# Optimization experiments

Hardware: AMD Instinct MI355X
Metric: run time of the kernel (lower is better)

The kernel has to match this reference:

```python
import jax, jax.numpy as jnp
import numpy as np

N = 50000        # nodes
E = 1_600_000    # edges (avg degree 32)
IN = 8           # in_channels
OUT = 64         # out_channels / hidden
K = 2            # Chebyshev order


def setup_inputs() -> dict:
    key = jax.random.key(0)
    ks = jax.random.split(key, 16)
    w = lambda k, s: (jax.random.normal(k, s, jnp.float32) * 0.05)
    inp = {
        "x": jax.random.normal(ks[0], (N, IN), jnp.float32),
        "H": jax.random.normal(ks[1], (N, OUT), jnp.float32),
        "edge_index": jax.random.randint(ks[2], (2, E), 0, N, dtype=jnp.int64),
    }
    names = [("z_x", IN), ("z_h", OUT), ("r_x", IN), ("r_h", OUT), ("c_x", IN), ("c_h", OUT)]
    for i, (nm, d) in enumerate(names):
        inp["W_" + nm] = w(ks[3 + 2 * i], (K, d, OUT))
        inp["b_" + nm] = w(ks[4 + 2 * i], (OUT,))
    return inp


def _cheb(x, W, b, row, col, norm):
    # PyG-style ChebConv with lambda_max=2: L_hat = -D^{-1/2} A D^{-1/2}
    # Tx0 = x; Tx1 = L_hat x; Tx_k = 2 L_hat Tx_{k-1} - Tx_{k-2}
    out = x @ W[0]
    Tx0 = x
    Tx1 = jax.ops.segment_sum(norm[:, None] * x[col], row, num_segments=N)
    out = out + Tx1 @ W[1]
    for k in range(2, W.shape[0]):
        Tx2 = 2.0 * jax.ops.segment_sum(norm[:, None] * Tx1[col], row, num_segments=N) - Tx0
        out = out + Tx2 @ W[k]
        Tx0, Tx1 = Tx1, Tx2
    return out + b


def reference(x, H, edge_index, W_z_x, b_z_x, W_z_h, b_z_h, W_r_x, b_r_x,
              W_r_h, b_r_h, W_c_x, b_c_x, W_c_h, b_c_h):
    row, col = edge_index[0], edge_index[1]
    deg = jax.ops.segment_sum(jnp.ones((E,), x.dtype), row, num_segments=N)
    dinv = jnp.where(deg > 0, 1.0 / jnp.sqrt(jnp.where(deg > 0, deg, 1.0)), 0.0)
    norm = -dinv[row] * dinv[col]  # sym-normalized, negated adjacency (L - I)

    Z = jax.nn.sigmoid(_cheb(x, W_z_x, b_z_x, row, col, norm)
                       + _cheb(H, W_z_h, b_z_h, row, col, norm))
    R = jax.nn.sigmoid(_cheb(x, W_r_x, b_r_x, row, col, norm)
                       + _cheb(H, W_r_h, b_r_h, row, col, norm))
    C = jnp.tanh(_cheb(x, W_c_x, b_c_x, row, col, norm)
                 + _cheb(R * H, W_c_h, b_c_h, row, col, norm))
    return Z * H + (1.0 - Z) * C
```

## Files before the change

### kernel.cpp

```cpp
#include <hip/hip_runtime.h>
#include <math.h>

#define IN_CH 8
#define OUT_CH 64

__global__ void deg_kernel(const int* __restrict__ row, int* __restrict__ deg, int E) {
    int i = blockIdx.x * blockDim.x + threadIdx.x;
    if (i < E) atomicAdd(&deg[row[i]], 1);
}

__global__ void dinv_kernel(const int* __restrict__ deg, float* __restrict__ dinv, int N) {
    int i = blockIdx.x * blockDim.x + threadIdx.x;
    if (i < N) {
        int d = deg[i];
        dinv[i] = (d > 0) ? rsqrtf((float)d) : 0.f;
    }
}

__global__ void scan_kernel(const int* __restrict__ deg, int* __restrict__ rowptr,
                            int* __restrict__ cursor, int N) {
    __shared__ int s_wave[17];
    __shared__ int s_running;
    int tid = threadIdx.x;
    int lane = tid & 63, wid = tid >> 6;
    if (tid == 0) s_running = 0;
    __syncthreads();
    for (int base = 0; base < N; base += 1024) {
        int i = base + tid;
        int v = (i < N) ? deg[i] : 0;
        int incl = v;
#pragma unroll
        for (int off = 1; off < 64; off <<= 1) {
            int t = __shfl_up(incl, off, 64);
            if (lane >= off) incl += t;
        }
        if (lane == 63) s_wave[wid] = incl;
        __syncthreads();
        if (wid == 0) {
            int wv = (lane < 16) ? s_wave[lane] : 0;
            int winc = wv;
#pragma unroll
            for (int off = 1; off < 16; off <<= 1) {
                int t = __shfl_up(winc, off, 64);
                if (lane >= off) winc += t;
            }
            if (lane < 16) s_wave[lane] = winc - wv;
            if (lane == 15) s_wave[16] = winc;
        }
        __syncthreads();
        int run = s_running;
        int excl = run + s_wave[wid] + incl - v;
        if (i < N) { rowptr[i] = excl; cursor[i] = excl; }
        __syncthreads();
        if (tid == 0) s_running = run + s_wave[16];
        __syncthreads();
    }
    if (tid == 0) rowptr[N] = s_running;
}

__global__ void bucket_kernel(const int* __restrict__ ei, const float* __restrict__ dinv,
                              int* __restrict__ cursor, int* __restrict__ col_s,
                              float* __restrict__ norm_s, int E) {
    int e = blockIdx.x * blockDim.x + threadIdx.x;
    if (e >= E) return;
    int r = ei[e];
    int c = ei[E + e];
    float nm = -dinv[r] * dinv[c];
    int pos = atomicAdd(&cursor[r], 1);
    col_s[pos] = c;
    norm_s[pos] = nm;
}

__global__ void gather64_kernel(const int* __restrict__ rowptr, const int* __restrict__ col_s,
                                const float* __restrict__ norm_s, const float* __restrict__ src,
                                float* __restrict__ dst, int N) {
    int n = blockIdx.x * (blockDim.x >> 6) + (threadIdx.x >> 6);
    int o = threadIdx.x & 63;
    if (n >= N) return;
    int beg = rowptr[n], end = rowptr[n + 1];
    float acc = 0.f;
#pragma unroll 4
    for (int j = beg; j < end; ++j) {
        int c = col_s[j];
        float nm = norm_s[j];
        acc = fmaf(nm, src[(long long)c * OUT_CH + o], acc);
    }
    dst[(long long)n * OUT_CH + o] = acc;
}

__global__ void gather8_kernel(const int* __restrict__ rowptr, const int* __restrict__ col_s,
                               const float* __restrict__ norm_s, const float* __restrict__ src,
                               float* __restrict__ dst, int N) {
    int n = blockIdx.x * (blockDim.x >> 6) + (threadIdx.x >> 6);
    int lane = threadIdx.x & 63;
    int g = lane >> 3;
    int o = lane & 7;
    if (n >= N) return;
    int beg = rowptr[n], end = rowptr[n + 1];
    float acc = 0.f;
    for (int j = beg + g; j < end; j += 8) {
        int c = col_s[j];
        float nm = norm_s[j];
        acc = fmaf(nm, src[(long long)c * IN_CH + o], acc);
    }
#pragma unroll
    for (int m = 8; m < 64; m <<= 1) acc += __shfl_xor(acc, m, 64);
    if (g == 0) dst[(long long)n * IN_CH + o] = acc;
}

__device__ __forceinline__ float sigmoidf(float v) { return 1.0f / (1.0f + expf(-v)); }

__global__ void gates_kernel(const float* __restrict__ x, const float* __restrict__ H,
                             const float* __restrict__ Lx, const float* __restrict__ LH,
                             const float* __restrict__ Wzx, const float* __restrict__ bzx,
                             const float* __restrict__ Wzh, const float* __restrict__ bzh,
                             const float* __restrict__ Wrx, const float* __restrict__ brx,
                             const float* __restrict__ Wrh, const float* __restrict__ brh,
                             float* __restrict__ Z, float* __restrict__ RH, int N) {
    int n = blockIdx.x * (blockDim.x >> 6) + (threadIdx.x >> 6);
    int o = threadIdx.x & 63;
    if (n >= N) return;
    float accZ = bzx[o] + bzh[o];
    float accR = brx[o] + brh[o];
    const float* xr  = x  + (long long)n * IN_CH;
    const float* lxr = Lx + (long long)n * IN_CH;
#pragma unroll
    for (int k = 0; k < IN_CH; ++k) {
        float xv = xr[k], lxv = lxr[k];
        accZ = fmaf(xv,  Wzx[k * 64 + o],       accZ);
        accZ = fmaf(lxv, Wzx[512 + k * 64 + o], accZ);
        accR = fmaf(xv,  Wrx[k * 64 + o],       accR);
        accR = fmaf(lxv, Wrx[512 + k * 64 + o], accR);
    }
    const float* hr  = H  + (long long)n * OUT_CH;
    const float* lhr = LH + (long long)n * OUT_CH;
    for (int k = 0; k < OUT_CH; ++k) {
        float hv = hr[k], lhv = lhr[k];
        accZ = fmaf(hv,  Wzh[k * 64 + o],        accZ);
        accZ = fmaf(lhv, Wzh[4096 + k * 64 + o], accZ);
        accR = fmaf(hv,  Wrh[k * 64 + o],        accR);
        accR = fmaf(lhv, Wrh[4096 + k * 64 + o], accR);
    }
    float z = sigmoidf(accZ);
    float r = sigmoidf(accR);
    Z[(long long)n * 64 + o]  = z;
    RH[(long long)n * 64 + o] = r * hr[o];
}

__global__ void final_kernel(const float* __restrict__ x, const float* __restrict__ H,
                             const float* __restrict__ Lx, const float* __restrict__ RH,
                             const float* __restrict__ LRH,
                             const float* __restrict__ Wcx, const float* __restrict__ bcx,
                             const float* __restrict__ Wch, const float* __restrict__ bch,
                             const float* __restrict__ Z, float* __restrict__ out, int N) {
    int n = blockIdx.x * (blockDim.x >> 6) + (threadIdx.x >> 6);
    int o = threadIdx.x & 63;
    if (n >= N) return;
    float accC = bcx[o] + bch[o];
    const float* xr  = x  + (long long)n * IN_CH;
    const float* lxr = Lx + (long long)n * IN_CH;
#pragma unroll
    for (int k = 0; k < IN_CH; ++k) {
        float xv = xr[k], lxv = lxr[k];
        accC = fmaf(xv,  Wcx[k * 64 + o],       accC);
        accC = fmaf(lxv, Wcx[512 + k * 64 + o], accC);
    }
    const float* rhr  = RH  + (long long)n * OUT_CH;
    const float* lrhr = LRH + (long long)n * OUT_CH;
    for (int k = 0; k < OUT_CH; ++k) {
        float rv = rhr[k], lrv = lrhr[k];
        accC = fmaf(rv,  Wch[k * 64 + o],        accC);
        accC = fmaf(lrv, Wch[4096 + k * 64 + o], accC);
    }
    float c = tanhf(accC);
    float z = Z[(long long)n * 64 + o];
    float h = H[(long long)n * 64 + o];
    out[(long long)n * 64 + o] = z * h + (1.0f - z) * c;
}

extern "C" void kernel_launch(void* const* d_in, const int* in_sizes, int n_in,
                              void* d_out, int out_size, void* d_ws, size_t ws_size,
                              hipStream_t stream) {
    const float* x   = (const float*)d_in[0];
    const float* H   = (const float*)d_in[1];
    const int*   ei  = (const int*)d_in[2];
    const float* Wzx = (const float*)d_in[3];
    const float* bzx = (const float*)d_in[4];
    const float* Wzh = (const float*)d_in[5];
    const float* bzh = (const float*)d_in[6];
    const float* Wrx = (const float*)d_in[7];
    const float* brx = (const float*)d_in[8];
    const float* Wrh = (const float*)d_in[9];
    const float* brh = (const float*)d_in[10];
    const float* Wcx = (const float*)d_in[11];
    const float* bcx = (const float*)d_in[12];
    const float* Wch = (const float*)d_in[13];
    const float* bch = (const float*)d_in[14];

    const int N = in_sizes[0] / IN_CH;
    const int E = in_sizes[2] / 2;

    int*   deg    = (int*)d_ws;
    float* dinv   = (float*)(deg + N);
    int*   rowptr = (int*)(dinv + N);
    int*   col_s  = rowptr + (N + 1);
    float* norm_s = (float*)(col_s + E);
    float* Lx     = norm_s + E;
    float* LH     = Lx + (size_t)N * IN_CH;
    float* Z      = LH + (size_t)N * OUT_CH;
    float* RH     = Z  + (size_t)N * OUT_CH;
    float* LRH    = LH;
    int*   cursor = deg;

    hipMemsetAsync(deg, 0, (size_t)N * sizeof(int), stream);

    const int tb = 256;
    deg_kernel<<<(E + tb - 1) / tb, tb, 0, stream>>>(ei, deg, E);
    dinv_kernel<<<(N + tb - 1) / tb, tb, 0, stream>>>(deg, dinv, N);
    scan_kernel<<<1, 1024, 0, stream>>>(deg, rowptr, cursor, N);
    bucket_kernel<<<(E + tb - 1) / tb, tb, 0, stream>>>(ei, dinv, cursor, col_s, norm_s, E);

    const int nblk = (N + 3) / 4;
    gather8_kernel <<<nblk, tb, 0, stream>>>(rowptr, col_s, norm_s, x, Lx, N);
    gather64_kernel<<<nblk, tb, 0, stream>>>(rowptr, col_s, norm_s, H, LH, N);

    gates_kernel<<<nblk, tb, 0, stream>>>(x, H, Lx, LH, Wzx, bzx, Wzh, bzh,
                                          Wrx, brx, Wrh, brh, Z, RH, N);

    gather64_kernel<<<nblk, tb, 0, stream>>>(rowptr, col_s, norm_s, RH, LRH, N);

    final_kernel<<<nblk, tb, 0, stream>>>(x, H, Lx, RH, LRH, Wcx, bcx, Wch, bch,
                                          Z, (float*)d_out, N);
}
```

Before: 714.5 us.

## Pack edge metadata as int2, broadcast via shuffles, register-block dense gate kernels

Edge column and norm are now stored interleaved as one int2 array. The 64-wide gather loads up to 64 edges' metadata cooperatively, one per lane, and broadcasts each with wave shuffles instead of every lane reloading the same scalars. The gate and final kernels now process 4 nodes per wave: node features are held in registers and broadcast with shuffles, so each weight load is reused across 4 nodes. This trades extra shuffle instructions and register pressure for fewer redundant global and scalar loads.

```diff
diff --git a/kernel.cpp b/kernel.cpp
--- a/kernel.cpp
+++ b/kernel.cpp
@@ -59,38 +59,38 @@
 }
 
 __global__ void bucket_kernel(const int* __restrict__ ei, const float* __restrict__ dinv,
-                              int* __restrict__ cursor, int* __restrict__ col_s,
-                              float* __restrict__ norm_s, int E) {
+                              int* __restrict__ cursor, int2* __restrict__ meta, int E) {
     int e = blockIdx.x * blockDim.x + threadIdx.x;
     if (e >= E) return;
     int r = ei[e];
     int c = ei[E + e];
     float nm = -dinv[r] * dinv[c];
     int pos = atomicAdd(&cursor[r], 1);
-    col_s[pos] = c;
-    norm_s[pos] = nm;
-}
-
-__global__ void gather64_kernel(const int* __restrict__ rowptr, const int* __restrict__ col_s,
-                                const float* __restrict__ norm_s, const float* __restrict__ src,
-                                float* __restrict__ dst, int N) {
+    meta[pos] = make_int2(c, __float_as_int(nm));
+}
+
+__global__ void gather64_kernel(const int* __restrict__ rowptr, const int2* __restrict__ meta,
+                                const float* __restrict__ src, float* __restrict__ dst, int N) {
     int n = blockIdx.x * (blockDim.x >> 6) + (threadIdx.x >> 6);
-    int o = threadIdx.x & 63;
+    int lane = threadIdx.x & 63;
     if (n >= N) return;
     int beg = rowptr[n], end = rowptr[n + 1];
     float acc = 0.f;
+    for (int base = beg; base < end; base += 64) {
+        int cnt = min(end - base, 64);
+        int2 m = meta[base + min(lane, cnt - 1)];
 #pragma unroll 4
-    for (int j = beg; j < end; ++j) {
-        int c = col_s[j];
-        float nm = norm_s[j];
-        acc = fmaf(nm, src[(long long)c * OUT_CH + o], acc);
-    }
-    dst[(long long)n * OUT_CH + o] = acc;
-}
-
-__global__ void gather8_kernel(const int* __restrict__ rowptr, const int* __restrict__ col_s,
-                               const float* __restrict__ norm_s, const float* __restrict__ src,
-                               float* __restrict__ dst, int N) {
+        for (int e = 0; e < cnt; ++e) {
+            int c = __shfl(m.x, e, 64);
+            float nm = __int_as_float(__shfl(m.y, e, 64));
+            acc = fmaf(nm, src[(size_t)c * OUT_CH + lane], acc);
+        }
+    }
+    dst[(size_t)n * OUT_CH + lane] = acc;
+}
+
+__global__ void gather8_kernel(const int* __restrict__ rowptr, const int2* __restrict__ meta,
+                               const float* __restrict__ src, float* __restrict__ dst, int N) {
     int n = blockIdx.x * (blockDim.x >> 6) + (threadIdx.x >> 6);
     int lane = threadIdx.x & 63;
     int g = lane >> 3;
@@ -99,83 +99,131 @@
     int beg = rowptr[n], end = rowptr[n + 1];
     float acc = 0.f;
     for (int j = beg + g; j < end; j += 8) {
-        int c = col_s[j];
-        float nm = norm_s[j];
-        acc = fmaf(nm, src[(long long)c * IN_CH + o], acc);
-    }
-#pragma unroll
-    for (int m = 8; m < 64; m <<= 1) acc += __shfl_xor(acc, m, 64);
-    if (g == 0) dst[(long long)n * IN_CH + o] = acc;
+        int2 m = meta[j];
+        acc = fmaf(__int_as_float(m.y), src[(size_t)m.x * IN_CH + o], acc);
+    }
+#pragma unroll
+    for (int msk = 8; msk < 64; msk <<= 1) acc += __shfl_xor(acc, msk, 64);
+    if (g == 0) dst[(size_t)n * IN_CH + o] = acc;
 }
 
 __device__ __forceinline__ float sigmoidf(float v) { return 1.0f / (1.0f + expf(-v)); }
 
-__global__ void gates_kernel(const float* __restrict__ x, const float* __restrict__ H,
-                             const float* __restrict__ Lx, const float* __restrict__ LH,
-                             const float* __restrict__ Wzx, const float* __restrict__ bzx,
-                             const float* __restrict__ Wzh, const float* __restrict__ bzh,
-                             const float* __restrict__ Wrx, const float* __restrict__ brx,
-                             const float* __restrict__ Wrh, const float* __restrict__ brh,
-                             float* __restrict__ Z, float* __restrict__ RH, int N) {
-    int n = blockIdx.x * (blockDim.x >> 6) + (threadIdx.x >> 6);
-    int o = threadIdx.x & 63;
-    if (n >= N) return;
-    float accZ = bzx[o] + bzh[o];
-    float accR = brx[o] + brh[o];
-    const float* xr  = x  + (long long)n * IN_CH;
-    const float* lxr = Lx + (long long)n * IN_CH;
+__global__ __launch_bounds__(256) void gates_kernel(
+        const float* __restrict__ x, const float* __restrict__ H,
+        const float* __restrict__ Lx, const float* __restrict__ LH,
+        const float* __restrict__ Wzx, const float* __restrict__ bzx,
+        const float* __restrict__ Wzh, const float* __restrict__ bzh,
+        const float* __restrict__ Wrx, const float* __restrict__ brx,
+        const float* __restrict__ Wrh, const float* __restrict__ brh,
+        float* __restrict__ Z, float* __restrict__ RH, int N) {
+    int wid = threadIdx.x >> 6;
+    int lane = threadIdx.x & 63;
+    int n0 = blockIdx.x * 16 + wid * 4;
+
+    float axl[4], hreg[4], lhreg[4], accZ[4], accR[4];
+    float bz = bzx[lane] + bzh[lane];
+    float br = brx[lane] + brh[lane];
+#pragma unroll
+    for (int i = 0; i < 4; ++i) {
+        int n = n0 + i;
+        int nn = (n < N) ? n : 0;
+        axl[i]   = (lane < 8) ? x[(size_t)nn * IN_CH + lane]
+                 : (lane < 16 ? Lx[(size_t)nn * IN_CH + (lane - 8)] : 0.f);
+        hreg[i]  = H[(size_t)nn * OUT_CH + lane];
+        lhreg[i] = LH[(size_t)nn * OUT_CH + lane];
+        accZ[i] = bz;
+        accR[i] = br;
+    }
 #pragma unroll
     for (int k = 0; k < IN_CH; ++k) {
-        float xv = xr[k], lxv = lxr[k];
-        accZ = fmaf(xv,  Wzx[k * 64 + o],       accZ);
-        accZ = fmaf(lxv, Wzx[512 + k * 64 + o], accZ);
-        accR = fmaf(xv,  Wrx[k * 64 + o],       accR);
-        accR = fmaf(lxv, Wrx[512 + k * 64 + o], accR);
-    }
-    const float* hr  = H  + (long long)n * OUT_CH;
-    const float* lhr = LH + (long long)n * OUT_CH;
+        float wz0 = Wzx[k * 64 + lane], wz1 = Wzx[512 + k * 64 + lane];
+        float wr0 = Wrx[k * 64 + lane], wr1 = Wrx[512 + k * 64 + lane];
+#pragma unroll
+        for (int i = 0; i < 4; ++i) {
+            float xv  = __shfl(axl[i], k, 64);
+            float lxv = __shfl(axl[i], k + 8, 64);
+            accZ[i] = fmaf(xv, wz0, fmaf(lxv, wz1, accZ[i]));
+            accR[i] = fmaf(xv, wr0, fmaf(lxv, wr1, accR[i]));
+        }
+    }
+#pragma unroll 8
     for (int k = 0; k < OUT_CH; ++k) {
-        float hv = hr[k], lhv = lhr[k];
-        accZ = fmaf(hv,  Wzh[k * 64 + o],        accZ);
-        accZ = fmaf(lhv, Wzh[4096 + k * 64 + o], accZ);
-        accR = fmaf(hv,  Wrh[k * 64 + o],        accR);
-        accR = fmaf(lhv, Wrh[4096 + k * 64 + o], accR);
-    }
-    float z = sigmoidf(accZ);
-    float r = sigmoidf(accR);
-    Z[(long long)n * 64 + o]  = z;
-    RH[(long long)n * 64 + o] = r * hr[o];
-}
-
-__global__ void final_kernel(const float* __restrict__ x, const float* __restrict__ H,
-                             const float* __restrict__ Lx, const float* __restrict__ RH,
-                             const float* __restrict__ LRH,
-                             const float* __restrict__ Wcx, const float* __restrict__ bcx,
-                             const float* __restrict__ Wch, const float* __restrict__ bch,
-                             const float* __restrict__ Z, float* __restrict__ out, int N) {
-    int n = blockIdx.x * (blockDim.x >> 6) + (threadIdx.x >> 6);
-    int o = threadIdx.x & 63;
-    if (n >= N) return;
-    float accC = bcx[o] + bch[o];
-    const float* xr  = x  + (long long)n * IN_CH;
-    const float* lxr = Lx + (long long)n * IN_CH;
+        float wh0 = Wzh[k * 64 + lane], wh1 = Wzh[4096 + k * 64 + lane];
+        float wr0 = Wrh[k * 64 + lane], wr1 = Wrh[4096 + k * 64 + lane];
+#pragma unroll
+        for (int i = 0; i < 4; ++i) {
+            float hv  = __shfl(hreg[i], k, 64);
+            float lhv = __shfl(lhreg[i], k, 64);
+            accZ[i] = fmaf(hv, wh0, fmaf(lhv, wh1, accZ[i]));
+            accR[i] = fmaf(hv, wr0, fmaf(lhv, wr1, accR[i]));
+        }
+    }
+#pragma unroll
+    for (int i = 0; i < 4; ++i) {
+        int n = n0 + i;
+        if (n < N) {
+            float z = sigmoidf(accZ[i]);
+            float r = sigmoidf(accR[i]);
+            Z[(size_t)n * OUT_CH + lane]  = z;
+            RH[(size_t)n * OUT_CH + lane] = r * hreg[i];
+        }
+    }
+}
+
+__global__ __launch_bounds__(256) void final_kernel(
+        const float* __restrict__ x, const float* __restrict__ H,
+        const float* __restrict__ Lx, const float* __restrict__ RH,
+        const float* __restrict__ LRH,
+        const float* __restrict__ Wcx, const float* __restrict__ bcx,
+        const float* __restrict__ Wch, const float* __restrict__ bch,
+        const float* __restrict__ Z, float* __restrict__ out, int N) {
+    int wid = threadIdx.x >> 6;
+    int lane = threadIdx.x & 63;
+    int n0 = blockIdx.x * 16 + wid * 4;
+
+    float axl[4], rhreg[4], lrhreg[4], accC[4];
+    float bc = bcx[lane] + bch[lane];
+#pragma unroll
+    for (int i = 0; i < 4; ++i) {
+        int n = n0 + i;
+        int nn = (n < N) ? n : 0;
+        axl[i]    = (lane < 8) ? x[(size_t)nn * IN_CH + lane]
+                  : (lane < 16 ? Lx[(size_t)nn * IN_CH + (lane - 8)] : 0.f);
+        rhreg[i]  = RH[(size_t)nn * OUT_CH + lane];
+        lrhreg[i] = LRH[(size_t)nn * OUT_CH + lane];
+        accC[i] = bc;
+    }
 #pragma unroll
     for (int k = 0; k < IN_CH; ++k) {
-        float xv = xr[k], lxv = lxr[k];
-        accC = fmaf(xv,  Wcx[k * 64 + o],       accC);
-        accC = fmaf(lxv, Wcx[512 + k * 64 + o], accC);
-    }
-    const float* rhr  = RH  + (long long)n * OUT_CH;
-    const float* lrhr = LRH + (long long)n * OUT_CH;
+        float wc0 = Wcx[k * 64 + lane], wc1 = Wcx[512 + k * 64 + lane];
+#pragma unroll
+        for (int i = 0; i < 4; ++i) {
+            float xv  = __shfl(axl[i], k, 64);
+            float lxv = __shfl(axl[i], k + 8, 64);
+            accC[i] = fmaf(xv, wc0, fmaf(lxv, wc1, accC[i]));
+        }
+    }
+#pragma unroll 8
     for (int k = 0; k < OUT_CH; ++k) {
-        float rv = rhr[k], lrv = lrhr[k];
-        accC = fmaf(rv,  Wch[k * 64 + o],        accC);
-        accC = fmaf(lrv, Wch[4096 + k * 64 + o], accC);
-    }
-    float c = tanhf(accC);
-    float z = Z[(long long)n * 64 + o];
-    float h = H[(long long)n * 64 + o];
-    out[(long long)n * 64 + o] = z * h + (1.0f - z) * c;
+        float wh0 = Wch[k * 64 + lane], wh1 = Wch[4096 + k * 64 + lane];
+#pragma unroll
+        for (int i = 0; i < 4; ++i) {
+            float rv  = __shfl(rhreg[i], k, 64);
+            float lrv = __shfl(lrhreg[i], k, 64);
+            accC[i] = fmaf(rv, wh0, fmaf(lrv, wh1, accC[i]));
+        }
+    }
+#pragma unroll
+    for (int i = 0; i < 4; ++i) {
+        int n = n0 + i;
+        if (n < N) {
+            float c = tanhf(accC[i]);
+            float z = Z[(size_t)n * OUT_CH + lane];
+            float h = H[(size_t)n * OUT_CH + lane];
+            out[(size_t)n * OUT_CH + lane] = z * h + (1.0f - z) * c;
+        }
+    }
 }
 
 extern "C" void kernel_launch(void* const* d_in, const int* in_sizes, int n_in,
@@ -203,9 +251,8 @@
     int*   deg    = (int*)d_ws;
     float* dinv   = (float*)(deg + N);
     int*   rowptr = (int*)(dinv + N);
-    int*   col_s  = rowptr + (N + 1);
-    float* norm_s = (float*)(col_s + E);
-    float* Lx     = norm_s + E;
+    int2*  meta   = (int2*)(rowptr + (N + 2));
+    float* Lx     = (float*)(meta + E);
     float* LH     = Lx + (size_t)N * IN_CH;
     float* Z      = LH + (size_t)N * OUT_CH;
     float* RH     = Z  + (size_t)N * OUT_CH;
@@ -218,17 +265,19 @@
     deg_kernel<<<(E + tb - 1) / tb, tb, 0, stream>>>(ei, deg, E);
     dinv_kernel<<<(N + tb - 1) / tb, tb, 0, stream>>>(deg, dinv, N);
     scan_kernel<<<1, 1024, 0, stream>>>(deg, rowptr, cursor, N);
-    bucket_kernel<<<(E + tb - 1) / tb, tb, 0, stream>>>(ei, dinv, cursor, col_s, norm_s, E);
-
-    const int nblk = (N + 3) / 4;
-    gather8_kernel <<<nblk, tb, 0, stream>>>(rowptr, col_s, norm_s, x, Lx, N);
-    gather64_kernel<<<nblk, tb, 0, stream>>>(rowptr, col_s, norm_s, H, LH, N);
-
-    gates_kernel<<<nblk, tb, 0, stream>>>(x, H, Lx, LH, Wzx, bzx, Wzh, bzh,
-                                          Wrx, brx, Wrh, brh, Z, RH, N);
-
-    gather64_kernel<<<nblk, tb, 0, stream>>>(rowptr, col_s, norm_s, RH, LRH, N);
-
-    final_kernel<<<nblk, tb, 0, stream>>>(x, H, Lx, RH, LRH, Wcx, bcx, Wch, bch,
-                                          Z, (float*)d_out, N);
-}
+    bucket_kernel<<<(E + tb - 1) / tb, tb, 0, stream>>>(ei, dinv, cursor, meta, E);
+
+    const int nblk4 = (N + 3) / 4;
+    const int nblk16 = (N + 15) / 16;
+
+    gather8_kernel <<<nblk4, tb, 0, stream>>>(rowptr, meta, x, Lx, N);
+    gather64_kernel<<<nblk4, tb, 0, stream>>>(rowptr, meta, H, LH, N);
+
+    gates_kernel<<<nblk16, tb, 0, stream>>>(x, H, Lx, LH, Wzx, bzx, Wzh, bzh,
+                                            Wrx, brx, Wrh, brh, Z, RH, N);
+
+    gather64_kernel<<<nblk4, tb, 0, stream>>>(rowptr, meta, RH, LRH, N);
+
+    final_kernel<<<nblk16, tb, 0, stream>>>(x, H, Lx, RH, LRH, Wcx, bcx, Wch, bch,
+                                            Z, (float*)d_out, N);
+}
```

Result: faster. 665.6 us (-6.8%).
